# Optimization experiments

Hardware: AMD Instinct MI355X
Metric: run time of the kernel (lower is better)

## Reference

```python
import jax, jax.numpy as jnp
import numpy as np

SAMPLE_RATE = 16000
HUM_FREQ = 60
Q_FACTOR = 30.0
BATCH = 128
SAMPLES = 160000


def _notch_sos(freq, Q, fs):
    # scipy.signal.iirnotch closed form (gb = 1/sqrt(2) -> beta = tan(bw/2))
    w0 = 2.0 * np.pi * freq / fs
    beta = np.tan(w0 / (2.0 * Q))
    gain = 1.0 / (1.0 + beta)
    b0 = gain
    b1 = -2.0 * gain * np.cos(w0)
    b2 = gain
    a1 = -2.0 * gain * np.cos(w0)
    a2 = 2.0 * gain - 1.0
    # tf2sos of a 2nd-order TF: single section [b0,b1,b2,a0=1,a1,a2]
    return [b0, b1, b2, 1.0, a1, a2]


def _build_sos():
    rows = []
    for f in (HUM_FREQ, HUM_FREQ * 2, HUM_FREQ * 3):
        if f < SAMPLE_RATE / 2:
            rows.append(_notch_sos(f, Q_FACTOR, SAMPLE_RATE))
    return np.asarray(rows, dtype=np.float32)  # [3, 6]


def setup_inputs() -> dict:
    key = jax.random.key(0)
    audio = jax.random.normal(key, (BATCH, SAMPLES), dtype=jnp.float32)
    sos = jnp.asarray(_build_sos())  # [n_sections, 6], a0 == 1
    return {"audio": audio, "sos": sos}


def _sosfilt(sos, x):
    """Cascaded biquad IIR (direct form II transposed), matching scipy.sosfilt.
    sos: [n_sections, 6] with a0 == 1.  x: [B, T].  Returns [B, T].
    """
    n_sections = sos.shape[0]
    B = x.shape[0]

    def step(z, xt):  # z: [n_sections, 2, B], xt: [B]
        y = xt
        new_z = []
        for s in range(n_sections):
            b0, b1, b2 = sos[s, 0], sos[s, 1], sos[s, 2]
            a1, a2 = sos[s, 4], sos[s, 5]
            out = b0 * y + z[s, 0]
            z0 = b1 * y - a1 * out + z[s, 1]
            z1 = b2 * y - a2 * out
            new_z.append(jnp.stack([z0, z1]))
            y = out
        return jnp.stack(new_z), y

    z_init = jnp.zeros((n_sections, 2, B), dtype=x.dtype)
    _, ys = jax.lax.scan(step, z_init, x.T)  # ys: [T, B]
    return ys.T


def reference(audio, sos):
    squeeze = audio.ndim == 1
    a = audio[None, :] if squeeze else audio
    y = _sosfilt(sos, a)
    return y[0] if squeeze else y
```

## Files before the change

### kernel.cpp

```cpp
#include <hip/hip_runtime.h>

typedef float vfloat4 __attribute__((ext_vector_type(4)));

#define B_ROWS 128
#define T_SAMP 160000
#define NSEC 3
#define LCH 20
#define NF4 5
#define RST 21
#define SUPW 1280
#define NSUP 125
#define NSC (B_ROWS * NSUP)
#define WPB 4

struct Coefs { float b0[NSEC], b1[NSEC], b2[NSEC], a1[NSEC], a2[NSEC]; };

__device__ __forceinline__ void load_coefs(const float* __restrict__ sos, Coefs& c) {
#pragma unroll
  for (int s = 0; s < NSEC; ++s) {
    c.b0[s] = sos[s * 6 + 0];
    c.b1[s] = sos[s * 6 + 1];
    c.b2[s] = sos[s * 6 + 2];
    c.a1[s] = sos[s * 6 + 4];
    c.a2[s] = sos[s * 6 + 5];
  }
}

__device__ __forceinline__ float df2t_step(const Coefs& c, float z[6], float x) {
  float y = x;
#pragma unroll
  for (int s = 0; s < NSEC; ++s) {
    float out = fmaf(c.b0[s], y, z[2 * s]);
    float t0  = fmaf(c.b1[s], y, z[2 * s + 1]);
    z[2 * s]     = fmaf(-c.a1[s], out, t0);
    float t1  = c.b2[s] * y;
    z[2 * s + 1] = fmaf(-c.a2[s], out, t1);
    y = out;
  }
  return y;
}

__device__ __forceinline__ void tri_combine(float f[6], const float* __restrict__ P,
                                            const float t[6]) {
  float nf[6];
#pragma unroll
  for (int e = 0; e < 6; ++e) {
    float acc = f[e];
    const int kmax = ((e >> 1) << 1) + 2;
#pragma unroll
    for (int kk = 0; kk < 6; ++kk)
      if (kk < kmax) acc = fmaf(P[e * 6 + kk], t[kk], acc);
    nf[e] = acc;
  }
#pragma unroll
  for (int e = 0; e < 6; ++e) f[e] = nf[e];
}

__device__ __forceinline__ float dmm6(float a, float b, int i, int j) {
  float s = 0.f;
#pragma unroll
  for (int k = 0; k < 6; ++k)
    s = fmaf(__shfl(a, i * 6 + k), __shfl(b, k * 6 + j), s);
  return s;
}

__global__ __launch_bounds__(64) void setup_kernel(const float* __restrict__ sos,
                                                   float* __restrict__ mats) {
  __shared__ float Ash[36];
  const int lane = threadIdx.x;
  Coefs cf; load_coefs(sos, cf);
  if (lane == 0) {
    float A[36];
#pragma unroll
    for (int jc = 0; jc < 6; ++jc) {
      float z[6] = {0.f, 0.f, 0.f, 0.f, 0.f, 0.f};
      z[jc] = 1.f;
      df2t_step(cf, z, 0.f);
#pragma unroll
      for (int ic = 0; ic < 6; ++ic) A[ic * 6 + jc] = z[ic];
    }
#pragma unroll
    for (int q = 0; q < 36; ++q) Ash[q] = A[q];
  }
  __syncthreads();

  const int e = (lane < 36) ? lane : 0;
  const int mi = e / 6, mj = e % 6;
  float a1p = Ash[e];
  float a2p  = dmm6(a1p, a1p, mi, mj);
  float a4p  = dmm6(a2p, a2p, mi, mj);
  float a8p  = dmm6(a4p, a4p, mi, mj);
  float a16p = dmm6(a8p, a8p, mi, mj);
  float pk = dmm6(a16p, a4p, mi, mj);
  if (lane < 36) mats[lane] = pk;
#pragma unroll
  for (int k = 1; k < 6; ++k) {
    pk = dmm6(pk, pk, mi, mj);
    if (lane < 36) mats[k * 36 + lane] = pk;
  }
  float q = dmm6(pk, pk, mi, mj);
  if (lane < 36) mats[216 + lane] = q;
#pragma unroll
  for (int k = 1; k < 7; ++k) {
    q = dmm6(q, q, mi, mj);
    if (lane < 36) mats[216 + k * 36 + lane] = q;
  }
}

__global__ __launch_bounds__(256) void pass1_kernel(const float* __restrict__ x,
                                                    const float* __restrict__ sos,
                                                    const float* __restrict__ mats,
                                                    float* __restrict__ Fsup) {
  const int tid = threadIdx.x, w = tid >> 6, lane = tid & 63;
  Coefs cf; load_coefs(sos, cf);
  const int S = blockIdx.x * WPB + w;
  const int r = S / NSUP, s = S - r * NSUP;
  const float4* src = reinterpret_cast<const float4*>(
      x + (size_t)r * T_SAMP + (size_t)s * SUPW + (size_t)lane * LCH);
  float4 v0 = src[0], v1 = src[1], v2 = src[2], v3 = src[3], v4 = src[4];

  float f[6] = {0.f, 0.f, 0.f, 0.f, 0.f, 0.f};
  df2t_step(cf, f, v0.x); df2t_step(cf, f, v0.y); df2t_step(cf, f, v0.z); df2t_step(cf, f, v0.w);
  df2t_step(cf, f, v1.x); df2t_step(cf, f, v1.y); df2t_step(cf, f, v1.z); df2t_step(cf, f, v1.w);
  df2t_step(cf, f, v2.x); df2t_step(cf, f, v2.y); df2t_step(cf, f, v2.z); df2t_step(cf, f, v2.w);
  df2t_step(cf, f, v3.x); df2t_step(cf, f, v3.y); df2t_step(cf, f, v3.z); df2t_step(cf, f, v3.w);
  df2t_step(cf, f, v4.x); df2t_step(cf, f, v4.y); df2t_step(cf, f, v4.z); df2t_step(cf, f, v4.w);

#pragma unroll
  for (int k = 0; k < 6; ++k) {
    float t6[6];
#pragma unroll
    for (int e = 0; e < 6; ++e) t6[e] = __shfl_up(f[e], 1 << k);
    if (lane >= (1 << k)) tri_combine(f, mats + k * 36, t6);
  }
  if (lane == 63) {
    float* fo = Fsup + (size_t)S * 6;
#pragma unroll
    for (int e = 0; e < 6; ++e) fo[e] = f[e];
  }
}

__global__ __launch_bounds__(64) void middle_scan(const float* __restrict__ Fsup,
                                                  const float* __restrict__ mats,
                                                  float* __restrict__ zsup) {
  const float* Qm = mats + 216;
  const int r = blockIdx.x, lane = threadIdx.x;
  const float* frow = Fsup + (size_t)r * NSUP * 6;
  float fc[2][6];
#pragma unroll
  for (int jj = 0; jj < 2; ++jj) {
    int c = 2 * lane + jj;
#pragma unroll
    for (int e = 0; e < 6; ++e) fc[jj][e] = (c < NSUP) ? frow[c * 6 + e] : 0.f;
  }
  float s[6] = {0.f, 0.f, 0.f, 0.f, 0.f, 0.f};
#pragma unroll
  for (int jj = 0; jj < 2; ++jj) {
    float ns[6];
#pragma unroll
    for (int e = 0; e < 6; ++e) {
      float acc = fc[jj][e];
#pragma unroll
      for (int kk = 0; kk < 6; ++kk) acc = fmaf(Qm[e * 6 + kk], s[kk], acc);
      ns[e] = acc;
    }
#pragma unroll
    for (int e = 0; e < 6; ++e) s[e] = ns[e];
  }
#pragma unroll
  for (int k = 0; k < 6; ++k) {
    float t[6];
#pragma unroll
    for (int e = 0; e < 6; ++e) t[e] = __shfl_up(s[e], 1 << k);
    if (lane >= (1 << k)) tri_combine(s, Qm + (k + 1) * 36, t);
  }
  float z[6];
#pragma unroll
  for (int e = 0; e < 6; ++e) {
    float t = __shfl_up(s[e], 1);
    z[e] = (lane == 0) ? 0.f : t;
  }
  float* zrow = zsup + (size_t)r * NSUP * 6;
#pragma unroll
  for (int jj = 0; jj < 2; ++jj) {
    int c = 2 * lane + jj;
    if (c < NSUP) {
#pragma unroll
      for (int e = 0; e < 6; ++e) zrow[c * 6 + e] = z[e];
    }
    float nz[6];
#pragma unroll
    for (int e = 0; e < 6; ++e) {
      float acc = fc[jj][e];
#pragma unroll
      for (int kk = 0; kk < 6; ++kk) acc = fmaf(Qm[e * 6 + kk], z[kk], acc);
      nz[e] = acc;
    }
#pragma unroll
    for (int e = 0; e < 6; ++e) z[e] = nz[e];
  }
}

__global__ __launch_bounds__(256) void pass2_kernel(const float* __restrict__ x,
                                                    const float* __restrict__ sos,
                                                    const float* __restrict__ mats,
                                                    const float* __restrict__ zsup,
                                                    float* __restrict__ y) {
  __shared__ float Tr[WPB][64 * RST];
  const int tid = threadIdx.x, w = tid >> 6, lane = tid & 63;
  Coefs cf; load_coefs(sos, cf);
  const int S = blockIdx.x * WPB + w;
  const int r = S / NSUP, s = S - r * NSUP;
  const size_t base = (size_t)r * T_SAMP + (size_t)s * SUPW;
  const float4* src = reinterpret_cast<const float4*>(x + base + (size_t)lane * LCH);
  float4 v0 = src[0], v1 = src[1], v2 = src[2], v3 = src[3], v4 = src[4];

  float z0[6];
  const float* zp = zsup + (size_t)S * 6;
#pragma unroll
  for (int e = 0; e < 6; ++e) z0[e] = zp[e];

  float f[6] = {0.f, 0.f, 0.f, 0.f, 0.f, 0.f};
  df2t_step(cf, f, v0.x); df2t_step(cf, f, v0.y); df2t_step(cf, f, v0.z); df2t_step(cf, f, v0.w);
  df2t_step(cf, f, v1.x); df2t_step(cf, f, v1.y); df2t_step(cf, f, v1.z); df2t_step(cf, f, v1.w);
  df2t_step(cf, f, v2.x); df2t_step(cf, f, v2.y); df2t_step(cf, f, v2.z); df2t_step(cf, f, v2.w);
  df2t_step(cf, f, v3.x); df2t_step(cf, f, v3.y); df2t_step(cf, f, v3.z); df2t_step(cf, f, v3.w);
  df2t_step(cf, f, v4.x); df2t_step(cf, f, v4.y); df2t_step(cf, f, v4.z); df2t_step(cf, f, v4.w);

  if (lane == 0) tri_combine(f, mats, z0);
#pragma unroll
  for (int k = 0; k < 6; ++k) {
    float t6[6];
#pragma unroll
    for (int e = 0; e < 6; ++e) t6[e] = __shfl_up(f[e], 1 << k);
    if (lane >= (1 << k)) tri_combine(f, mats + k * 36, t6);
  }
  float zs[6];
#pragma unroll
  for (int e = 0; e < 6; ++e) {
    float tt = __shfl_up(f[e], 1);
    zs[e] = (lane == 0) ? z0[e] : tt;
  }

  float* myrow = &Tr[w][lane * RST];
  myrow[0]  = df2t_step(cf, zs, v0.x); myrow[1]  = df2t_step(cf, zs, v0.y);
  myrow[2]  = df2t_step(cf, zs, v0.z); myrow[3]  = df2t_step(cf, zs, v0.w);
  myrow[4]  = df2t_step(cf, zs, v1.x); myrow[5]  = df2t_step(cf, zs, v1.y);
  myrow[6]  = df2t_step(cf, zs, v1.z); myrow[7]  = df2t_step(cf, zs, v1.w);
  myrow[8]  = df2t_step(cf, zs, v2.x); myrow[9]  = df2t_step(cf, zs, v2.y);
  myrow[10] = df2t_step(cf, zs, v2.z); myrow[11] = df2t_step(cf, zs, v2.w);
  myrow[12] = df2t_step(cf, zs, v3.x); myrow[13] = df2t_step(cf, zs, v3.y);
  myrow[14] = df2t_step(cf, zs, v3.z); myrow[15] = df2t_step(cf, zs, v3.w);
  myrow[16] = df2t_step(cf, zs, v4.x); myrow[17] = df2t_step(cf, zs, v4.y);
  myrow[18] = df2t_step(cf, zs, v4.z); myrow[19] = df2t_step(cf, zs, v4.w);
  __syncthreads();

  float* dst = y + base;
#pragma unroll
  for (int i2 = 0; i2 < NF4; ++i2) {
    int q = i2 * 64 + lane, k = q / NF4, m = q - k * NF4;
    vfloat4 w4;
    w4.x = Tr[w][k * RST + m * 4 + 0];
    w4.y = Tr[w][k * RST + m * 4 + 1];
    w4.z = Tr[w][k * RST + m * 4 + 2];
    w4.w = Tr[w][k * RST + m * 4 + 3];
    __builtin_nontemporal_store(w4, reinterpret_cast<vfloat4*>(dst + 4 * q));
  }
}

extern "C" void kernel_launch(void* const* d_in, const int* in_sizes, int n_in,
                              void* d_out, int out_size, void* d_ws, size_t ws_size,
                              hipStream_t stream) {
  const float* x = (const float*)d_in[0];
  const float* sos = (const float*)d_in[1];
  float* y = (float*)d_out;

  float* Fsup = (float*)d_ws;
  float* zsup = Fsup + (size_t)NSC * 6;
  float* mats = zsup + (size_t)NSC * 6;

  hipLaunchKernelGGL(setup_kernel, dim3(1), dim3(64), 0, stream, sos, mats);
  hipLaunchKernelGGL(pass1_kernel, dim3(NSC / WPB), dim3(256), 0, stream, x, sos, mats, Fsup);
  hipLaunchKernelGGL(middle_scan, dim3(B_ROWS), dim3(64), 0, stream, Fsup, mats, zsup);
  hipLaunchKernelGGL(pass2_kernel, dim3(NSC / WPB), dim3(256), 0, stream, x, sos, mats, zsup, y);
}
```

Baseline: 63.28 us.

## Replace second filter pass with zero-state output plus precomputed state-response correction

Pass 2 used to run the full cascaded biquad recurrence twice per chunk: once from zero state to get the chunk's end state, then again from the true initial state to produce outputs. Now the zero-state outputs from the first run are kept, and the effect of the incoming state is added through a precomputed 20x6 output-response table (g * A^t), built in setup_kernel by binary powering of the stored A powers. Each output then costs 6 FMAs that do not depend on one another, instead of a serial recurrence of about 15 dependent ops, which shortens the dependency chain. The cost is 480 extra floats of table loaded per thread from global/L1, plus some floating-point rounding differences.

Measured after the change: 63.70 us (median of 2 runs). No clear change (+0.7%).

```diff
diff --git a/kernel.cpp b/kernel.cpp
--- a/kernel.cpp
+++ b/kernel.cpp
@@ -67,6 +67,7 @@
 __global__ __launch_bounds__(64) void setup_kernel(const float* __restrict__ sos,
                                                    float* __restrict__ mats) {
   __shared__ float Ash[36];
+  __shared__ float As5[5 * 36];
   const int lane = threadIdx.x;
   Coefs cf; load_coefs(sos, cf);
   if (lane == 0) {
@@ -91,6 +92,10 @@
   float a4p  = dmm6(a2p, a2p, mi, mj);
   float a8p  = dmm6(a4p, a4p, mi, mj);
   float a16p = dmm6(a8p, a8p, mi, mj);
+  if (lane < 36) {
+    As5[lane] = a1p; As5[36 + lane] = a2p; As5[72 + lane] = a4p;
+    As5[108 + lane] = a8p; As5[144 + lane] = a16p;
+  }
   float pk = dmm6(a16p, a4p, mi, mj);
   if (lane < 36) mats[lane] = pk;
 #pragma unroll
@@ -104,6 +109,26 @@
   for (int k = 1; k < 7; ++k) {
     q = dmm6(q, q, mi, mj);
     if (lane < 36) mats[216 + k * 36 + lane] = q;
+  }
+  if (lane < LCH) {
+    float g[6] = {cf.b0[1] * cf.b0[2], 0.f, cf.b0[2], 0.f, 1.f, 0.f};
+#pragma unroll
+    for (int k = 0; k < 5; ++k) {
+      if (lane & (1 << k)) {
+        float ng[6];
+#pragma unroll
+        for (int j = 0; j < 6; ++j) {
+          float acc = 0.f;
+#pragma unroll
+          for (int i = 0; i < 6; ++i) acc = fmaf(g[i], As5[k * 36 + i * 6 + j], acc);
+          ng[j] = acc;
+        }
+#pragma unroll
+        for (int j = 0; j < 6; ++j) g[j] = ng[j];
+      }
+    }
+#pragma unroll
+    for (int j = 0; j < 6; ++j) mats[468 + lane * 6 + j] = g[j];
   }
 }
 
@@ -221,11 +246,16 @@
   for (int e = 0; e < 6; ++e) z0[e] = zp[e];
 
   float f[6] = {0.f, 0.f, 0.f, 0.f, 0.f, 0.f};
-  df2t_step(cf, f, v0.x); df2t_step(cf, f, v0.y); df2t_step(cf, f, v0.z); df2t_step(cf, f, v0.w);
-  df2t_step(cf, f, v1.x); df2t_step(cf, f, v1.y); df2t_step(cf, f, v1.z); df2t_step(cf, f, v1.w);
-  df2t_step(cf, f, v2.x); df2t_step(cf, f, v2.y); df2t_step(cf, f, v2.z); df2t_step(cf, f, v2.w);
-  df2t_step(cf, f, v3.x); df2t_step(cf, f, v3.y); df2t_step(cf, f, v3.z); df2t_step(cf, f, v3.w);
-  df2t_step(cf, f, v4.x); df2t_step(cf, f, v4.y); df2t_step(cf, f, v4.z); df2t_step(cf, f, v4.w);
+  v0.x = df2t_step(cf, f, v0.x); v0.y = df2t_step(cf, f, v0.y);
+  v0.z = df2t_step(cf, f, v0.z); v0.w = df2t_step(cf, f, v0.w);
+  v1.x = df2t_step(cf, f, v1.x); v1.y = df2t_step(cf, f, v1.y);
+  v1.z = df2t_step(cf, f, v1.z); v1.w = df2t_step(cf, f, v1.w);
+  v2.x = df2t_step(cf, f, v2.x); v2.y = df2t_step(cf, f, v2.y);
+  v2.z = df2t_step(cf, f, v2.z); v2.w = df2t_step(cf, f, v2.w);
+  v3.x = df2t_step(cf, f, v3.x); v3.y = df2t_step(cf, f, v3.y);
+  v3.z = df2t_step(cf, f, v3.z); v3.w = df2t_step(cf, f, v3.w);
+  v4.x = df2t_step(cf, f, v4.x); v4.y = df2t_step(cf, f, v4.y);
+  v4.z = df2t_step(cf, f, v4.z); v4.w = df2t_step(cf, f, v4.w);
 
   if (lane == 0) tri_combine(f, mats, z0);
 #pragma unroll
@@ -242,17 +272,19 @@
     zs[e] = (lane == 0) ? z0[e] : tt;
   }
 
+  const float* Gm = mats + 468;
   float* myrow = &Tr[w][lane * RST];
-  myrow[0]  = df2t_step(cf, zs, v0.x); myrow[1]  = df2t_step(cf, zs, v0.y);
-  myrow[2]  = df2t_step(cf, zs, v0.z); myrow[3]  = df2t_step(cf, zs, v0.w);
-  myrow[4]  = df2t_step(cf, zs, v1.x); myrow[5]  = df2t_step(cf, zs, v1.y);
-  myrow[6]  = df2t_step(cf, zs, v1.z); myrow[7]  = df2t_step(cf, zs, v1.w);
-  myrow[8]  = df2t_step(cf, zs, v2.x); myrow[9]  = df2t_step(cf, zs, v2.y);
-  myrow[10] = df2t_step(cf, zs, v2.z); myrow[11] = df2t_step(cf, zs, v2.w);
-  myrow[12] = df2t_step(cf, zs, v3.x); myrow[13] = df2t_step(cf, zs, v3.y);
-  myrow[14] = df2t_step(cf, zs, v3.z); myrow[15] = df2t_step(cf, zs, v3.w);
-  myrow[16] = df2t_step(cf, zs, v4.x); myrow[17] = df2t_step(cf, zs, v4.y);
-  myrow[18] = df2t_step(cf, zs, v4.z); myrow[19] = df2t_step(cf, zs, v4.w);
+  auto corr = [&](int tl, float yz) {
+    float a = yz;
+#pragma unroll
+    for (int e = 0; e < 6; ++e) a = fmaf(Gm[tl * 6 + e], zs[e], a);
+    myrow[tl] = a;
+  };
+  corr(0, v0.x);  corr(1, v0.y);  corr(2, v0.z);  corr(3, v0.w);
+  corr(4, v1.x);  corr(5, v1.y);  corr(6, v1.z);  corr(7, v1.w);
+  corr(8, v2.x);  corr(9, v2.y);  corr(10, v2.z); corr(11, v2.w);
+  corr(12, v3.x); corr(13, v3.y); corr(14, v3.z); corr(15, v3.w);
+  corr(16, v4.x); corr(17, v4.y); corr(18, v4.z); corr(19, v4.w);
   __syncthreads();
 
   float* dst = y + base;
```
